# Optimization experiments

Measured on AMD Instinct MI355X. Metric: run time of the kernel, lower is better.

Reference implementation:

```python
import jax, jax.numpy as jnp
import numpy as np

B = 32      # graphs per batch
N_NODES = 1024  # nodes per graph
K = 16      # top-k edges per node


def setup_inputs() -> dict:
    key = jax.random.key(0)
    k1, k2 = jax.random.split(key)
    x = jax.random.normal(k1, (B * N_NODES, 128), dtype=jnp.float32) * 0.1
    W = jax.random.normal(k2, (128, 64), dtype=jnp.float32) * (1.0 / np.sqrt(128))
    b = jnp.zeros((64,), dtype=jnp.float32)
    temperature = jnp.asarray(4.0, dtype=jnp.float32)
    return {"x": x, "W": W, "b": b, "temperature": temperature}


def reference(x, W, b, temperature):
    # Encoder: linear node embedding. out: [B*n, C]
    out = x @ W + b
    C = out.shape[-1]
    # Per-graph features, detached as in the original (graph_x = out[...].detach())
    h = jax.lax.stop_gradient(out).reshape(B, N_NODES, C)
    # Pairwise squared euclidean distances per graph: d[b,i,j] = ||h_i - h_j||^2
    sq = jnp.sum(h * h, axis=-1)  # [B, n]
    d_e = sq[:, :, None] + sq[:, None, :] - 2.0 * jnp.einsum('bic,bjc->bij', h, h)
    logits = jnp.exp(-temperature * d_e)  # [B, n, n]
    # Gumbel-noised top-k edge sampling
    z = jax.random.gumbel(jax.random.key(1), logits.shape, logits.dtype)
    _, edges_hat = jax.lax.top_k(logits + z, K)  # [B, n, K] int32
    # Build global edge index with cumulative per-graph node offsets
    offsets = (jnp.arange(B, dtype=jnp.int32) * N_NODES)[:, None, None]  # [B,1,1]
    rows = jnp.broadcast_to(jnp.arange(N_NODES, dtype=jnp.int32)[None, :, None] + offsets,
                            (B, N_NODES, K))
    cols = edges_hat.astype(jnp.int32) + offsets
    edges_idx = jnp.stack((rows.reshape(-1), cols.reshape(-1)))  # [2, B*n*K]
    return out, edges_idx
```

## Files before the change

kernel.cpp:

```cpp
#include <hip/hip_runtime.h>
#include <math.h>

#define OUT_ELEMS 2097152
#define EDGE_ELEMS 524288

__device__ __forceinline__ unsigned int rotl32(unsigned int x, int r){
  return (x << r) | (x >> (32 - r));
}

__device__ __forceinline__ unsigned int tf_bits_part(unsigned int e){
  unsigned int x0 = 0u, x1 = e;
  const unsigned int ks1 = 1u;
  const unsigned int ks2 = 0x1BD11BDBu;
  x1 += ks1;
#define TFR(r) { x0 += x1; x1 = rotl32(x1, r); x1 ^= x0; }
  TFR(13) TFR(15) TFR(26) TFR(6)
  x0 += ks1; x1 += ks2 + 1u;
  TFR(17) TFR(29) TFR(16) TFR(24)
  x0 += ks2; x1 += 0u + 2u;
  TFR(13) TFR(15) TFR(26) TFR(6)
  x0 += 0u;  x1 += ks1 + 3u;
  TFR(17) TFR(29) TFR(16) TFR(24)
  x0 += ks1; x1 += ks2 + 4u;
  TFR(13) TFR(15) TFR(26) TFR(6)
  x0 += ks2; x1 += 0u + 5u;
#undef TFR
  return x0 ^ x1;
}

__device__ __forceinline__ double rcp64(double x){
  double r;
  asm("v_rcp_f64 %0, %1" : "=v"(r) : "v"(x));
  double e = fma(-x, r, 1.0); r = fma(r, e, r);
  e = fma(-x, r, 1.0); r = fma(r, e, r);
  return r;
}

__device__ __forceinline__ double fast_exp(double x){
  double fn = __builtin_rint(x * 1.4426950408889634);
  int n = (int)fn;
  double r = fma(fn, -0.6931471803691238, x);
  r = fma(fn, -1.9082149292705877e-10, r);
  double p = 2.7557319223985893e-06;
  p = fma(r, p, 2.4801587301587302e-05);
  p = fma(r, p, 1.9841269841269841e-04);
  p = fma(r, p, 1.3888888888888889e-03);
  p = fma(r, p, 8.3333333333333333e-03);
  p = fma(r, p, 4.1666666666666664e-02);
  p = fma(r, p, 1.6666666666666666e-01);
  p = fma(r, p, 0.5);
  p = fma(r, p, 1.0);
  p = fma(r, p, 1.0);
  double scale = __longlong_as_double(((long long)(n + 1023)) << 52);
  return p * scale;
}

__device__ __forceinline__ double fast_log(double x){
  long long bx = __double_as_longlong(x);
  long long e = (bx >> 52) - 1023;
  double m = __longlong_as_double((bx & 0xFFFFFFFFFFFFFll) |
                                  0x3FF0000000000000ll);
  int big = m > 1.4142135623730951;
  m = big ? 0.5 * m : m;
  e += big;
  double s = (m - 1.0) * rcp64(m + 1.0);
  double s2 = s * s;
  double p = fma(s2, 2.0/11.0, 2.0/9.0);
  p = fma(s2, p, 2.0/7.0);
  p = fma(s2, p, 2.0/5.0);
  p = fma(s2, p, 2.0/3.0);
  double lm = fma(s * s2, p, 2.0 * s);
  return fma((double)e, 0.6931471805599453, lm);
}

__device__ __forceinline__ unsigned long long score_cand(
    const float* __restrict__ og, const double* __restrict__ hrow,
    unsigned int jc, unsigned int base, double Td, bool act){
  const float4* cp4 = (const float4*)(og + ((size_t)jc << 6));
  double acc = 0.0;
  #pragma unroll 4
  for (int ch = 0; ch < 16; ++ch){
    float4 cf = cp4[ch];
    double d0 = hrow[(ch << 2) + 0] - (double)cf.x;
    double d1 = hrow[(ch << 2) + 1] - (double)cf.y;
    double d2 = hrow[(ch << 2) + 2] - (double)cf.z;
    double d3 = hrow[(ch << 2) + 3] - (double)cf.w;
    acc = fma(d0, d0, acc);
    acc = fma(d1, d1, acc);
    acc = fma(d2, d2, acc);
    acc = fma(d3, d3, acc);
  }
  if (!act) return 0ull;
  double sgm = fast_exp(-Td * acc);
  unsigned int bits = tf_bits_part(base | jc);
  float f = __uint_as_float(0x3f800000u | (bits >> 9)) - 1.0f;
  double u = (f > 0.0f) ? (double)f : 1.1754943508222875e-38;
  double w = -fast_log(u);
  double z = -fast_log(w);
  double sc = sgm + z;
  unsigned long long kb = (unsigned long long)__double_as_longlong(sc);
  kb ^= (unsigned long long)(((long long)kb) >> 63) | 0x8000000000000000ull;
  return (kb & ~1023ull) | (unsigned long long)(1023u - jc);
}

__device__ __forceinline__ unsigned long long bitonic64_desc(
    unsigned long long key, int lane){
  #pragma unroll
  for (int k = 2; k <= 64; k <<= 1){
    #pragma unroll
    for (int j = k >> 1; j; j >>= 1){
      unsigned long long o = __shfl_xor(key, j, 64);
      bool keep_hi = ((lane & k) == 0) == ((lane & j) == 0);
      key = (keep_hi == (o > key)) ? o : key;
    }
  }
  return key;
}

__device__ __forceinline__ unsigned int bitonic32_desc(
    unsigned int key, int lane){
  #pragma unroll
  for (int k = 2; k <= 64; k <<= 1){
    #pragma unroll
    for (int j = k >> 1; j; j >>= 1){
      unsigned int o = __shfl_xor(key, j, 64);
      bool keep_hi = ((lane & k) == 0) == ((lane & j) == 0);
      key = (keep_hi == (o > key)) ? o : key;
    }
  }
  return key;
}

__global__ __launch_bounds__(256) void encoder_v10(
    const float* __restrict__ x, const float* __restrict__ W,
    const float* __restrict__ b, float* __restrict__ out){
  __shared__ double xs64[8192];
  const int tid = threadIdx.x;
  const int w = tid >> 6, c = tid & 63;
  const size_t r0 = (size_t)blockIdx.x << 6;

  {
    const float4* xg4 = (const float4*)(x + (r0 << 7));
    #pragma unroll
    for (int s = 0; s < 8; ++s){
      const int idx = tid + (s << 8);
      float4 v = xg4[idx];
      double2 d0, d1;
      d0.x = (double)v.x; d0.y = (double)v.y;
      d1.x = (double)v.z; d1.y = (double)v.w;
      *(double2*)&xs64[(idx << 2) + 0] = d0;
      *(double2*)&xs64[(idx << 2) + 2] = d1;
    }
  }
  __syncthreads();

  double acc[16];
  const double bc = (double)b[c];
  #pragma unroll
  for (int i = 0; i < 16; ++i) acc[i] = bc;

  #pragma unroll 4
  for (int k = 0; k < 128; k += 4){
    const double w0 = (double)W[((k + 0) << 6) + c];
    const double w1 = (double)W[((k + 1) << 6) + c];
    const double w2 = (double)W[((k + 2) << 6) + c];
    const double w3 = (double)W[((k + 3) << 6) + c];
    #pragma unroll
    for (int i = 0; i < 16; ++i){
      const double2 xa = *(const double2*)&xs64[(((w << 4) + i) << 7) + k];
      const double2 xb = *(const double2*)&xs64[(((w << 4) + i) << 7) + k + 2];
      acc[i] = fma(xa.x, w0, acc[i]);
      acc[i] = fma(xa.y, w1, acc[i]);
      acc[i] = fma(xb.x, w2, acc[i]);
      acc[i] = fma(xb.y, w3, acc[i]);
    }
  }
  #pragma unroll
  for (int i = 0; i < 16; ++i)
    out[((r0 + (w << 4) + i) << 6) + c] = (float)acc[i];
}

__global__ __launch_bounds__(256, 8) void edges_v10(
    const float* __restrict__ out32, const float* __restrict__ temp,
    float* __restrict__ rows_out, float* __restrict__ cols_out){
  __shared__ double hid[4][64];
  __shared__ unsigned int cl[4][128];
  const int tid = threadIdx.x, wave = tid >> 6, lane = tid & 63;
  const int gb = blockIdx.x >> 8;
  const int i0 = (blockIdx.x & 255) << 2;
  const int r  = i0 + wave;
  const float* __restrict__ og = out32 + ((size_t)gb << 16);

  hid[wave][lane] = (double)og[((size_t)r << 6) + lane];

  const unsigned int base = ((unsigned int)gb << 20) | ((unsigned int)r << 10);

  unsigned int v[16];
  unsigned int pmax = 0u;
  #pragma unroll
  for (int m = 0; m < 16; ++m){
    const unsigned int j = (unsigned int)(m << 6) + (unsigned int)lane;
    unsigned int bits = tf_bits_part(base | j);
    v[m] = (bits & ~1023u) | (1023u - j);
    pmax = (v[m] > pmax) ? v[m] : pmax;
  }

  unsigned int sorted = bitonic32_desc(pmax, lane);
  unsigned int b16p = __shfl(sorted, 15, 64);

  float u16 = __uint_as_float(0x3f800000u | (b16p >> 9)) - 1.0f;
  float z16 = -__logf(-__logf(u16));
  float uc  = __expf(-__expf(-(z16 - 1.001f)));
  unsigned int cp = ((__float_as_uint(1.0f + uc) & 0x7FFFFFu) << 9) & ~1023u;

  int cnt = 0;
  #pragma unroll
  for (int m = 0; m < 16; ++m) cnt += (v[m] >= cp) ? 1 : 0;
  int s = cnt;
  #pragma unroll
  for (int off = 1; off < 64; off <<= 1){
    int o = __shfl_up(s, off, 64);
    s += (lane >= off) ? o : 0;
  }
  int nc = __shfl(s, 63, 64);
  nc = (nc > 128) ? 128 : nc;
  int slot = s - cnt;
  #pragma unroll
  for (int m = 0; m < 16; ++m){
    if (v[m] >= cp && slot < 128){
      cl[wave][slot] = 1023u - (v[m] & 1023u);
      ++slot;
    }
  }

  const double Td = (double)temp[0];
  const bool act1 = (lane < nc);
  unsigned int jc1 = act1 ? cl[wave][lane] : 0u;
  unsigned long long key = score_cand(og, hid[wave], jc1, base, Td, act1);
  key = bitonic64_desc(key, lane);

  if (nc > 64){
    const int idx2 = 64 + lane;
    const bool act2 = (idx2 < nc);
    unsigned int jc2 = act2 ? cl[wave][idx2] : 0u;
    unsigned long long k2 = score_cand(og, hid[wave], jc2, base, Td, act2);
    k2 = bitonic64_desc(k2, lane);
    unsigned long long kr = __shfl(k2, 63 - lane, 64);
    key = (kr > key) ? kr : key;
    #pragma unroll
    for (int j = 32; j; j >>= 1){
      unsigned long long o = __shfl_xor(key, j, 64);
      bool left = (lane & j) == 0;
      bool take = left ? (o > key) : (o < key);
      key = take ? o : key;
    }
  }

  const int grow = (gb << 10) + r;
  if (lane < 16){
    rows_out[((size_t)grow << 4) + lane] = (float)grow;
    cols_out[((size_t)grow << 4) + lane] =
        (float)((gb << 10) + (1023 - (int)(key & 1023ull)));
  }
}

extern "C" void kernel_launch(void* const* d_in, const int* in_sizes, int n_in,
                              void* d_out, int out_size, void* d_ws, size_t ws_size,
                              hipStream_t stream){
  const float* x = (const float*)d_in[0];
  const float* W = (const float*)d_in[1];
  const float* b = (const float*)d_in[2];
  const float* T = (const float*)d_in[3];
  float* out      = (float*)d_out;
  float* rows_out = out + OUT_ELEMS;
  float* cols_out = rows_out + EDGE_ELEMS;

  encoder_v10<<<512, 256, 0, stream>>>(x, W, b, out);
  edges_v10<<<8192, 256, 0, stream>>>(out, T, rows_out, cols_out);
}
```

Baseline: 195.1 us.

## Drop shared-memory staging in encoder and read x rows directly per wave

```diff
diff --git a/kernel.cpp b/kernel.cpp
--- a/kernel.cpp
+++ b/kernel.cpp
@@ -131,56 +131,34 @@
   return key;
 }
 
-__global__ __launch_bounds__(256) void encoder_v10(
+__global__ __launch_bounds__(256) void encoder_v11(
     const float* __restrict__ x, const float* __restrict__ W,
     const float* __restrict__ b, float* __restrict__ out){
-  __shared__ double xs64[8192];
   const int tid = threadIdx.x;
-  const int w = tid >> 6, c = tid & 63;
-  const size_t r0 = (size_t)blockIdx.x << 6;
-
-  {
-    const float4* xg4 = (const float4*)(x + (r0 << 7));
-    #pragma unroll
-    for (int s = 0; s < 8; ++s){
-      const int idx = tid + (s << 8);
-      float4 v = xg4[idx];
-      double2 d0, d1;
-      d0.x = (double)v.x; d0.y = (double)v.y;
-      d1.x = (double)v.z; d1.y = (double)v.w;
-      *(double2*)&xs64[(idx << 2) + 0] = d0;
-      *(double2*)&xs64[(idx << 2) + 2] = d1;
-    }
-  }
-  __syncthreads();
-
-  double acc[16];
+  const int wu  = __builtin_amdgcn_readfirstlane(tid >> 6);
+  const int c   = tid & 63;
+  const size_t r0 = ((size_t)blockIdx.x << 5) + ((size_t)wu << 3);
+  const float* __restrict__ xr = x + (r0 << 7);
+
+  double acc[8];
   const double bc = (double)b[c];
   #pragma unroll
-  for (int i = 0; i < 16; ++i) acc[i] = bc;
+  for (int i = 0; i < 8; ++i) acc[i] = bc;
 
   #pragma unroll 4
-  for (int k = 0; k < 128; k += 4){
-    const double w0 = (double)W[((k + 0) << 6) + c];
-    const double w1 = (double)W[((k + 1) << 6) + c];
-    const double w2 = (double)W[((k + 2) << 6) + c];
-    const double w3 = (double)W[((k + 3) << 6) + c];
-    #pragma unroll
-    for (int i = 0; i < 16; ++i){
-      const double2 xa = *(const double2*)&xs64[(((w << 4) + i) << 7) + k];
-      const double2 xb = *(const double2*)&xs64[(((w << 4) + i) << 7) + k + 2];
-      acc[i] = fma(xa.x, w0, acc[i]);
-      acc[i] = fma(xa.y, w1, acc[i]);
-      acc[i] = fma(xb.x, w2, acc[i]);
-      acc[i] = fma(xb.y, w3, acc[i]);
-    }
-  }
-  #pragma unroll
-  for (int i = 0; i < 16; ++i)
-    out[((r0 + (w << 4) + i) << 6) + c] = (float)acc[i];
-}
-
-__global__ __launch_bounds__(256, 8) void edges_v10(
+  for (int k = 0; k < 128; ++k){
+    const double wk = (double)W[(k << 6) + c];
+    #pragma unroll
+    for (int i = 0; i < 8; ++i)
+      acc[i] = fma((double)xr[((size_t)i << 7) + k], wk, acc[i]);
+  }
+
+  #pragma unroll
+  for (int i = 0; i < 8; ++i)
+    out[((r0 + i) << 6) + c] = (float)acc[i];
+}
+
+__global__ __launch_bounds__(256, 8) void edges_v11(
     const float* __restrict__ out32, const float* __restrict__ temp,
     float* __restrict__ rows_out, float* __restrict__ cols_out){
   __shared__ double hid[4][64];
@@ -275,6 +253,6 @@
   float* rows_out = out + OUT_ELEMS;
   float* cols_out = rows_out + EDGE_ELEMS;
 
-  encoder_v10<<<512, 256, 0, stream>>>(x, W, b, out);
-  edges_v10<<<8192, 256, 0, stream>>>(out, T, rows_out, cols_out);
-}
+  encoder_v11<<<1024, 256, 0, stream>>>(x, W, b, out);
+  edges_v11<<<8192, 256, 0, stream>>>(out, T, rows_out, cols_out);
+}
```

Measured after the change: 197.1 us. Within noise of the previous version (+1.0%).
